# Kernel optimization log

Hardware: AMD Instinct MI355X
Metric: run time of the kernel (lower is better)

The kernel has to match this reference:

```python
import jax, jax.numpy as jnp
import numpy as np

N = 8_388_608  # total flattened scalar parameters across the model
K = 64         # VQ codebook size (dim = 1 -> scalar quantization)
W_STD = 0.02   # typical init std for MLP weights


def setup_inputs() -> dict:
    key = jax.random.key(0)
    k1, k2 = jax.random.split(key)
    weights = jax.random.normal(k1, (N,), dtype=jnp.float32) * W_STD
    codebook = jax.random.normal(k2, (K,), dtype=jnp.float32) * W_STD
    return {"weights": weights, "codebook": codebook}


def reference(weights, codebook):
    # VectorQuantize with dim=1: squared L2 distance of each scalar weight to
    # each scalar code, argmin, replace with nearest code (cdist+argmin+lookup).
    # dist[n, k] = (w_n - c_k)^2  -> [N, K]
    dist = (weights[:, None] - codebook[None, :]) ** 2
    idx = jnp.argmin(dist, axis=1)           # [N] nearest code index
    quantized = codebook[idx]                # [N] codebook replacement
    # straight-through estimator (as in vector-quantize-pytorch)
    return weights + jax.lax.stop_gradient(quantized - weights)
```

## Files before the change

### kernel.cpp

```cpp
#include <hip/hip_runtime.h>


#define VQ_K 64
#define TPB  256
#define SEG  4
#define BLK_F4 (TPB * SEG)

__global__ __launch_bounds__(TPB) void vq_kernel(
    const float* __restrict__ w,
    const float* __restrict__ cb,
    float* __restrict__ out,
    int n4)
{
    __shared__ float C[VQ_K];
    __shared__ float S[VQ_K + 2];
    __shared__ int   SI[VQ_K + 2];
    __shared__ float T2r[64];
    __shared__ float T1r[68];

    const int tid = threadIdx.x;

    if (tid < VQ_K) C[tid] = cb[tid];
    __syncthreads();
    if (tid < VQ_K) {
        const float c = C[tid];
        int rank = 0;
#pragma unroll
        for (int j = 0; j < VQ_K; ++j) {
            const float cj = C[j];
            rank += (cj < c || (cj == c && j < tid)) ? 1 : 0;
        }
        S[rank + 1] = c;
        SI[rank + 1] = tid;
    }
    if (tid == TPB - 1) {
        S[0] = __builtin_inff();          SI[0] = 1 << 30;
        S[VQ_K + 1] = __builtin_inff();   SI[VQ_K + 1] = 1 << 30;
    }
    __syncthreads();
    if (tid < 64) T2r[tid] = S[4 * (tid & 15) + 2];
    if (tid < 34) T1r[tid]      = (tid < 33) ? S[2 * tid + 1] : 0.0f;
    else if (tid < 68) { int i = tid - 34; T1r[tid] = (i < 33) ? S[2 * i + 1] : 0.0f; }
    __syncthreads();

    const float c32 = S[32];
    const float c16 = S[16], c48 = S[48];
    const float c8  = S[8],  c24 = S[24], c40 = S[40], c56 = S[56];
    const float c4  = S[4],  c12 = S[12], c20 = S[20], c28 = S[28];
    const float c36 = S[36], c44 = S[44], c52 = S[52], c60 = S[60];

    const int lane  = tid & 63;
    const int repl2 = lane & 48;
    const int repl1 = (lane >> 5) * 34;

    const int base4 = blockIdx.x * BLK_F4 + tid;
    float4 x[SEG];
    bool   ok[SEG];
#pragma unroll
    for (int s = 0; s < SEG; ++s) {
        const int i4 = base4 + s * TPB;
        ok[s] = (i4 < n4);
        if (ok[s]) x[s] = reinterpret_cast<const float4*>(w)[i4];
    }

#pragma unroll
    for (int s = 0; s < SEG; ++s) {
        if (!ok[s]) continue;
        float e[4] = {x[s].x, x[s].y, x[s].z, x[s].w};
        float r[4];
#pragma unroll
        for (int j = 0; j < 4; ++j) {
            const float wv = e[j];
            const bool b0 = (c32 <= wv);
            const float p1 = b0 ? c48 : c16;
            const bool b1 = (p1 <= wv);
            const float pa = b0 ? c56 : c24, pb = b0 ? c40 : c8;
            const float p2 = b1 ? pa : pb;
            const bool b2 = (p2 <= wv);
            const float q0 = b0 ? c36 : c4;
            const float q1 = b0 ? c44 : c12;
            const float q2 = b0 ? c52 : c20;
            const float q3 = b0 ? c60 : c28;
            const float r0 = b1 ? q2 : q0;
            const float r1 = b1 ? q3 : q1;
            const float p3 = b2 ? r1 : r0;
            const bool b3 = (p3 <= wv);
            const int i2 = (b0 ? 8 : 0) + (b1 ? 4 : 0) + (b2 ? 2 : 0) + (b3 ? 1 : 0);
            const float p4 = T2r[repl2 + i2];
            const bool b4 = (p4 <= wv);
            const int i1 = 2 * i2 + (b4 ? 1 : 0);
            const float p5 = T1r[repl1 + i1];
            const bool b5 = (p5 <= wv);
            const int pos = 2 * i1 + (b5 ? 1 : 0);

            const float cl = S[pos], cr = S[pos + 1];
            const float dl = wv - cl, dr = wv - cr;
            const float dl2 = dl * dl, dr2 = dr * dr;
            float q = (dr2 < dl2) ? cr : cl;
            const bool tie = (dl2 == dr2);
            if (__any(tie)) {
                if (tie) q = (SI[pos] < SI[pos + 1]) ? cl : cr;
            }
            r[j] = q;
        }
        const int i4 = base4 + s * TPB;
        reinterpret_cast<float4*>(out)[i4] = make_float4(r[0], r[1], r[2], r[3]);
    }
}

__global__ void vq_tail_kernel(const float* __restrict__ w,
                               const float* __restrict__ cb,
                               float* __restrict__ out, int start, int n) {
    int i = start + blockIdx.x * blockDim.x + threadIdx.x;
    if (i >= n) return;
    float wx = w[i];
    float c0 = cb[0], d0 = wx - c0;
    float bd = d0 * d0, bv = c0;
#pragma unroll
    for (int k = 1; k < VQ_K; ++k) {
        float c = cb[k], d = wx - c, dd = d * d;
        bool lt = dd < bd;
        bd = lt ? dd : bd;
        bv = lt ? c : bv;
    }
    out[i] = bv;
}

extern "C" void kernel_launch(void* const* d_in, const int* in_sizes, int n_in,
                              void* d_out, int out_size, void* d_ws, size_t ws_size,
                              hipStream_t stream) {
    const float* w  = (const float*)d_in[0];
    const float* cb = (const float*)d_in[1];
    float* out = (float*)d_out;
    const int n  = in_sizes[0];
    const int n4 = n / 4;

    if (n4 > 0) {
        const int grid = (n4 + BLK_F4 - 1) / BLK_F4;
        vq_kernel<<<grid, TPB, 0, stream>>>(w, cb, out, n4);
    }
    if (n4 * 4 < n) {
        vq_tail_kernel<<<1, 64, 0, stream>>>(w, cb, out, n4 * 4, n);
    }
}
```

Baseline: 21.98 us.

## Replace binary-search codebook lookup with bucketed hash table in LDS

Replaces the six-level binary search over the sorted codebook with a uniform 2048-bucket table over the codebook range. Each bucket stores up to four candidate codes, so a weight needs one float4 LDS read plus two compares, and a brute-force fallback handles overfull buckets and ties. Work per block is also doubled (SEG 4 to 8) to spread the larger per-block setup: histogram, scan and a 32KB table build. The cost is more shared memory and setup per block, which lowers occupancy in a kernel that is mostly memory-bound.

```diff
diff --git a/kernel.cpp b/kernel.cpp
--- a/kernel.cpp
+++ b/kernel.cpp
@@ -2,9 +2,16 @@
 
 
 #define VQ_K 64
+#define NB   2048
 #define TPB  256
-#define SEG  4
+#define SEG  8
 #define BLK_F4 (TPB * SEG)
+
+__device__ __forceinline__ int vq_key(float x, float lo, float inv) {
+    float t = (x - lo) * inv;
+    t = fminf(fmaxf(t, 0.0f), (float)(NB - 1));
+    return (int)t;
+}
 
 __global__ __launch_bounds__(TPB) void vq_kernel(
     const float* __restrict__ w,
@@ -12,16 +19,21 @@
     float* __restrict__ out,
     int n4)
 {
-    __shared__ float C[VQ_K];
-    __shared__ float S[VQ_K + 2];
-    __shared__ int   SI[VQ_K + 2];
-    __shared__ float T2r[64];
-    __shared__ float T1r[68];
+    __shared__ float  C[VQ_K];
+    __shared__ float  S[VQ_K + 4];
+    __shared__ float4 T[NB];
+    __shared__ unsigned int H[NB / 4];
+    __shared__ int    P[TPB];
+    __shared__ int    Q[TPB / 64];
 
     const int tid = threadIdx.x;
+    const float INF = __builtin_inff();
 
     if (tid < VQ_K) C[tid] = cb[tid];
+    H[2 * tid]     = 0u;
+    H[2 * tid + 1] = 0u;
     __syncthreads();
+
     if (tid < VQ_K) {
         const float c = C[tid];
         int rank = 0;
@@ -31,27 +43,65 @@
             rank += (cj < c || (cj == c && j < tid)) ? 1 : 0;
         }
         S[rank + 1] = c;
-        SI[rank + 1] = tid;
     }
-    if (tid == TPB - 1) {
-        S[0] = __builtin_inff();          SI[0] = 1 << 30;
-        S[VQ_K + 1] = __builtin_inff();   SI[VQ_K + 1] = 1 << 30;
+    if (tid == 0) S[0] = INF;
+    if (tid >= 1 && tid <= 3) S[VQ_K + tid] = INF;
+    __syncthreads();
+
+    const float lo  = S[1];
+    const float hi  = S[VQ_K];
+    const float inv = (hi > lo) ? ((float)NB / (hi - lo)) : 0.0f;
+
+    if (tid < VQ_K) {
+        const int k = vq_key(S[tid + 1], lo, inv);
+        atomicAdd(&H[k >> 2], 1u << ((k & 3) * 8));
     }
     __syncthreads();
-    if (tid < 64) T2r[tid] = S[4 * (tid & 15) + 2];
-    if (tid < 34) T1r[tid]      = (tid < 33) ? S[2 * tid + 1] : 0.0f;
-    else if (tid < 68) { int i = tid - 34; T1r[tid] = (i < 33) ? S[2 * i + 1] : 0.0f; }
+
+    const unsigned int h01 = H[2 * tid], h23 = H[2 * tid + 1];
+    int h[8], e[8];
+    {
+        int run = 0;
+#pragma unroll
+        for (int j = 0; j < 8; ++j) {
+            const unsigned int word = (j < 4) ? h01 : h23;
+            h[j] = (int)((word >> ((j & 3) * 8)) & 0xFFu);
+            e[j] = run;
+            run += h[j];
+        }
+        P[tid] = run;
+    }
     __syncthreads();
 
-    const float c32 = S[32];
-    const float c16 = S[16], c48 = S[48];
-    const float c8  = S[8],  c24 = S[24], c40 = S[40], c56 = S[56];
-    const float c4  = S[4],  c12 = S[12], c20 = S[20], c28 = S[28];
-    const float c36 = S[36], c44 = S[44], c52 = S[52], c60 = S[60];
+    int val = P[tid];
+    const int lane = tid & 63;
+#pragma unroll
+    for (int d = 1; d < 64; d <<= 1) {
+        int u = __shfl_up(val, d, 64);
+        if (lane >= d) val += u;
+    }
+    if (lane == 63) Q[tid >> 6] = val;
+    __syncthreads();
+    int base = val - P[tid];
+    {
+        const int wid = tid >> 6;
+        for (int i = 0; i < wid; ++i) base += Q[i];
+    }
 
-    const int lane  = tid & 63;
-    const int repl2 = lane & 48;
-    const int repl1 = (lane >> 5) * 34;
+    const float NANF = __uint_as_float(0x7fc00000u);
+#pragma unroll
+    for (int j = 0; j < 8; ++j) {
+        const int k  = tid * 8 + j;
+        const int p0 = base + e[j];
+        float4 ent;
+        if (h[j] >= 3) {
+            ent = make_float4(NANF, NANF, NANF, NANF);
+        } else {
+            ent = make_float4(S[p0], S[p0 + 1], S[p0 + 2], S[p0 + 3]);
+        }
+        T[k] = ent;
+    }
+    __syncthreads();
 
     const int base4 = blockIdx.x * BLK_F4 + tid;
     float4 x[SEG];
@@ -66,45 +116,40 @@
 #pragma unroll
     for (int s = 0; s < SEG; ++s) {
         if (!ok[s]) continue;
-        float e[4] = {x[s].x, x[s].y, x[s].z, x[s].w};
+        float ex[4] = {x[s].x, x[s].y, x[s].z, x[s].w};
         float r[4];
 #pragma unroll
         for (int j = 0; j < 4; ++j) {
-            const float wv = e[j];
-            const bool b0 = (c32 <= wv);
-            const float p1 = b0 ? c48 : c16;
-            const bool b1 = (p1 <= wv);
-            const float pa = b0 ? c56 : c24, pb = b0 ? c40 : c8;
-            const float p2 = b1 ? pa : pb;
-            const bool b2 = (p2 <= wv);
-            const float q0 = b0 ? c36 : c4;
-            const float q1 = b0 ? c44 : c12;
-            const float q2 = b0 ? c52 : c20;
-            const float q3 = b0 ? c60 : c28;
-            const float r0 = b1 ? q2 : q0;
-            const float r1 = b1 ? q3 : q1;
-            const float p3 = b2 ? r1 : r0;
-            const bool b3 = (p3 <= wv);
-            const int i2 = (b0 ? 8 : 0) + (b1 ? 4 : 0) + (b2 ? 2 : 0) + (b3 ? 1 : 0);
-            const float p4 = T2r[repl2 + i2];
-            const bool b4 = (p4 <= wv);
-            const int i1 = 2 * i2 + (b4 ? 1 : 0);
-            const float p5 = T1r[repl1 + i1];
-            const bool b5 = (p5 <= wv);
-            const int pos = 2 * i1 + (b5 ? 1 : 0);
-
-            const float cl = S[pos], cr = S[pos + 1];
+            const float wv = ex[j];
+            const int k = vq_key(wv, lo, inv);
+            const float4 ent = T[k];
+            const bool s1 = (ent.y <= wv);
+            const bool s2 = (ent.z <= wv);
+            const float cl = s2 ? ent.z : (s1 ? ent.y : ent.x);
+            const float cr = s2 ? ent.w : (s1 ? ent.z : ent.y);
             const float dl = wv - cl, dr = wv - cr;
             const float dl2 = dl * dl, dr2 = dr * dr;
             float q = (dr2 < dl2) ? cr : cl;
-            const bool tie = (dl2 == dr2);
-            if (__any(tie)) {
-                if (tie) q = (SI[pos] < SI[pos + 1]) ? cl : cr;
+            const bool bad = (q != q) || (dl2 == dr2 && cl != cr);
+            if (__any(bad)) {
+                if (bad) {
+                    float c0 = C[0];
+                    float d0 = wv - c0;
+                    float bd = d0 * d0, bv = c0;
+#pragma unroll 1
+                    for (int kk = 1; kk < VQ_K; ++kk) {
+                        float c = C[kk], d = wv - c, dd = d * d;
+                        bool lt = dd < bd;
+                        bd = lt ? dd : bd;
+                        bv = lt ? c : bv;
+                    }
+                    q = bv;
+                }
             }
             r[j] = q;
         }
-        const int i4 = base4 + s * TPB;
-        reinterpret_cast<float4*>(out)[i4] = make_float4(r[0], r[1], r[2], r[3]);
+        reinterpret_cast<float4*>(out)[base4 + s * TPB] =
+            make_float4(r[0], r[1], r[2], r[3]);
     }
 }
 
```

Measured after the change: 29.41 us. 33.8% more time.
